# Performance work log

Measured on AMD Instinct MI355X. Metric: run time of the kernel, lower is better.

The kernel has to match this reference:

```python
import jax, jax.numpy as jnp
import numpy as np

B_, N, C, H = 8192, 49, 192, 6
HD = C // H
SCALE = HD ** -0.5


def setup_inputs() -> dict:
    key = jax.random.key(0)
    k0, k1, k2, k3 = jax.random.split(key, 4)
    x = jax.random.normal(k0, (B_, N, C), dtype=jnp.float32)
    mask = jax.random.randint(k1, (B_, N), 0, 2, dtype=jnp.int32)
    w_qkv = jax.random.normal(k2, (C, 3 * C), dtype=jnp.float32) * 0.02
    b_qkv = jnp.zeros((3 * C,), dtype=jnp.float32)
    w_proj = jax.random.normal(k3, (C, C), dtype=jnp.float32) * 0.02
    b_proj = jnp.zeros((C,), dtype=jnp.float32)
    return {"x": x, "mask": mask, "w_qkv": w_qkv, "b_qkv": b_qkv,
            "w_proj": w_proj, "b_proj": b_proj}


def reference(x, mask, w_qkv, b_qkv, w_proj, b_proj):
    # qkv projection: [B_, N, 3C] -> [3, B_, H, N, HD]
    qkv = (x @ w_qkv + b_qkv).reshape(B_, N, 3, H, HD).transpose(2, 0, 3, 1, 4)
    q, k, v = qkv[0], qkv[1], qkv[2]
    # scaled QK^T: [B_, H, N, N]
    attn = jnp.einsum('bhnd,bhmd->bhnm', q, k) * SCALE
    # additive key mask: mask==0 positions get -inf
    attn = jnp.where(mask[:, None, None, :] == 0, -jnp.inf, attn)
    p = jax.nn.softmax(attn, axis=-1)  # dropout p=0 -> identity
    out = jnp.einsum('bhnm,bhmd->bhnd', p, v)  # AV
    out = out.transpose(0, 2, 1, 3).reshape(B_, N, C)
    return out @ w_proj + b_proj
```

## Files before the change

kernel.cpp:

```cpp
#include <hip/hip_runtime.h>


typedef __attribute__((ext_vector_type(8))) short short8;
typedef __attribute__((ext_vector_type(4))) float f32x4;

#define SCALE 0.17677669529663687f

__device__ __forceinline__ unsigned short f2bf(float x) {
    union { float f; unsigned int i; } v; v.f = x;
    return (unsigned short)((v.i + 0x7FFFu + ((v.i >> 16) & 1u)) >> 16);
}

__global__ void repack_qkv_kernel(const float* __restrict__ w,
                                  unsigned short* __restrict__ wp) {
    int idx = blockIdx.x * 256 + threadIdx.x;
    if (idx >= 6 * 576 * 32) return;
    int kk  = idx & 31;
    int col = (idx >> 5) % 576;
    int kt  = idx / (576 * 32);
    wp[idx] = f2bf(w[(kt * 32 + kk) * 576 + col]);
}

__global__ void repack_proj_kernel(const float* __restrict__ w,
                                   unsigned short* __restrict__ wp) {
    int idx = blockIdx.x * 256 + threadIdx.x;
    if (idx >= 6 * 192 * 32) return;
    int kk  = idx & 31;
    int col = (idx >> 5) % 192;
    int kt  = idx / (192 * 32);
    wp[idx] = f2bf(w[(kt * 32 + kk) * 192 + col]);
}

__global__ __launch_bounds__(384)
void win_attn_kernel(const float* __restrict__ x,
                     const int* __restrict__ mask,
                     const float* __restrict__ bqkv,
                     const float* __restrict__ bproj,
                     const unsigned short* __restrict__ wq,
                     const unsigned short* __restrict__ wpj,
                     float* __restrict__ out) {
    __shared__ __align__(16) unsigned short region[44544];
    __shared__ float mbias[64];

    const int b    = blockIdx.x;
    const int tid  = threadIdx.x;
    const int lane = tid & 63;
    const int h    = tid >> 6;
    const int quad = lane >> 4;
    const int l16  = lane & 15;

    const float* xb = x + (size_t)b * 9408;
    for (int i4 = tid; i4 < 2352; i4 += 384) {
        int flat = i4 * 4;
        int n = flat / 192, c = flat % 192;
        float4 v = *(const float4*)(const void*)&xb[flat];
        ushort4 pk = make_ushort4(f2bf(v.x), f2bf(v.y), f2bf(v.z), f2bf(v.w));
        *(ushort4*)(void*)&region[n * 200 + c] = pk;
    }
    if (tid < 375) {
        uint4 z = {0u, 0u, 0u, 0u};
        *(uint4*)(void*)&region[9800 + tid * 8] = z;
    }
    if (tid < 64)
        mbias[tid] = (tid < 49 && mask[b * 49 + tid] != 0) ? 0.0f : -1e30f;
    __syncthreads();

    f32x4 acc[6][4];
    #pragma unroll
    for (int t = 0; t < 6; ++t)
        #pragma unroll
        for (int mt = 0; mt < 4; ++mt)
            acc[t][mt] = (f32x4){0.f, 0.f, 0.f, 0.f};

    int colb[6];
    #pragma unroll
    for (int t = 0; t < 6; ++t) colb[t] = (t >> 1) * 192 + h * 32 + (t & 1) * 16;

    #pragma unroll
    for (int kt = 0; kt < 6; ++kt) {
        short8 af[4];
        #pragma unroll
        for (int mt = 0; mt < 4; ++mt)
            af[mt] = *(const short8*)(const void*)
                     &region[(mt * 16 + l16) * 200 + kt * 32 + quad * 8];
        #pragma unroll
        for (int t = 0; t < 6; ++t) {
            short8 bw = *(const short8*)(const void*)
                        &wq[(size_t)(kt * 576 + colb[t] + l16) * 32 + quad * 8];
            #pragma unroll
            for (int mt = 0; mt < 4; ++mt)
                acc[t][mt] = __builtin_amdgcn_mfma_f32_16x16x32_bf16(
                                 af[mt], bw, acc[t][mt], 0, 0, 0);
        }
    }
    #pragma unroll
    for (int t = 0; t < 6; ++t) {
        float bv = bqkv[colb[t] + l16];
        #pragma unroll
        for (int mt = 0; mt < 4; ++mt)
            #pragma unroll
            for (int r = 0; r < 4; ++r)
                acc[t][mt][r] += bv;
    }
    __syncthreads();

    unsigned short* qb  = &region[h * 7424];
    unsigned short* kb  = qb + 2560;
    unsigned short* vtb = qb + 5120;
    #pragma unroll
    for (int t = 0; t < 2; ++t)
        #pragma unroll
        for (int mt = 0; mt < 4; ++mt)
            #pragma unroll
            for (int r = 0; r < 4; ++r) {
                int row = mt * 16 + quad * 4 + r;
                qb[row * 40 + t * 16 + l16] = f2bf(acc[t    ][mt][r]);
                kb[row * 40 + t * 16 + l16] = f2bf(acc[t + 2][mt][r]);
            }
    #pragma unroll
    for (int t = 0; t < 2; ++t)
        #pragma unroll
        for (int mt = 0; mt < 4; ++mt) {
            int d = t * 16 + l16;
            ushort4 pk = make_ushort4(f2bf(acc[4 + t][mt][0]), f2bf(acc[4 + t][mt][1]),
                                      f2bf(acc[4 + t][mt][2]), f2bf(acc[4 + t][mt][3]));
            *(ushort4*)(void*)&vtb[d * 72 + mt * 16 + quad * 4] = pk;
        }

    f32x4 s[4][4];
    #pragma unroll
    for (int mt = 0; mt < 4; ++mt)
        #pragma unroll
        for (int nt = 0; nt < 4; ++nt)
            s[mt][nt] = (f32x4){0.f, 0.f, 0.f, 0.f};

    {
        short8 aq[4], bk[4];
        #pragma unroll
        for (int mt = 0; mt < 4; ++mt)
            aq[mt] = *(const short8*)(const void*)&qb[(mt * 16 + l16) * 40 + quad * 8];
        #pragma unroll
        for (int nt = 0; nt < 4; ++nt)
            bk[nt] = *(const short8*)(const void*)&kb[(nt * 16 + l16) * 40 + quad * 8];
        #pragma unroll
        for (int mt = 0; mt < 4; ++mt)
            #pragma unroll
            for (int nt = 0; nt < 4; ++nt)
                s[mt][nt] = __builtin_amdgcn_mfma_f32_16x16x32_bf16(
                                aq[mt], bk[nt], s[mt][nt], 0, 0, 0);
    }

    float mb[4];
    #pragma unroll
    for (int nt = 0; nt < 4; ++nt) mb[nt] = mbias[nt * 16 + l16];

    #pragma unroll
    for (int mt = 0; mt < 4; ++mt) {
        #pragma unroll
        for (int r = 0; r < 4; ++r) {
            float v0 = s[mt][0][r] * SCALE + mb[0];
            float v1 = s[mt][1][r] * SCALE + mb[1];
            float v2 = s[mt][2][r] * SCALE + mb[2];
            float v3 = s[mt][3][r] * SCALE + mb[3];
            float mx = fmaxf(fmaxf(v0, v1), fmaxf(v2, v3));
            mx = fmaxf(mx, __shfl_xor(mx, 1));
            mx = fmaxf(mx, __shfl_xor(mx, 2));
            mx = fmaxf(mx, __shfl_xor(mx, 4));
            mx = fmaxf(mx, __shfl_xor(mx, 8));
            float e0 = __expf(v0 - mx), e1 = __expf(v1 - mx);
            float e2 = __expf(v2 - mx), e3 = __expf(v3 - mx);
            float sum = e0 + e1 + e2 + e3;
            sum += __shfl_xor(sum, 1);
            sum += __shfl_xor(sum, 2);
            sum += __shfl_xor(sum, 4);
            sum += __shfl_xor(sum, 8);
            float inv = 1.0f / sum;
            s[mt][0][r] = e0 * inv; s[mt][1][r] = e1 * inv;
            s[mt][2][r] = e2 * inv; s[mt][3][r] = e3 * inv;
        }
    }

    unsigned short* pb = qb;
    #pragma unroll
    for (int mt = 0; mt < 4; ++mt)
        #pragma unroll
        for (int nt = 0; nt < 4; ++nt)
            #pragma unroll
            for (int r = 0; r < 4; ++r)
                pb[(mt * 16 + quad * 4 + r) * 72 + nt * 16 + l16] = f2bf(s[mt][nt][r]);

    f32x4 o[4][2];
    #pragma unroll
    for (int mt = 0; mt < 4; ++mt)
        #pragma unroll
        for (int dt = 0; dt < 2; ++dt)
            o[mt][dt] = (f32x4){0.f, 0.f, 0.f, 0.f};

    #pragma unroll
    for (int kt = 0; kt < 2; ++kt) {
        short8 ap[4], bv[2];
        #pragma unroll
        for (int mt = 0; mt < 4; ++mt)
            ap[mt] = *(const short8*)(const void*)
                     &pb[(mt * 16 + l16) * 72 + kt * 32 + quad * 8];
        #pragma unroll
        for (int dt = 0; dt < 2; ++dt)
            bv[dt] = *(const short8*)(const void*)
                     &vtb[(dt * 16 + l16) * 72 + kt * 32 + quad * 8];
        #pragma unroll
        for (int mt = 0; mt < 4; ++mt)
            #pragma unroll
            for (int dt = 0; dt < 2; ++dt)
                o[mt][dt] = __builtin_amdgcn_mfma_f32_16x16x32_bf16(
                                ap[mt], bv[dt], o[mt][dt], 0, 0, 0);
    }

    __syncthreads();
    #pragma unroll
    for (int dt = 0; dt < 2; ++dt)
        #pragma unroll
        for (int mt = 0; mt < 4; ++mt)
            #pragma unroll
            for (int r = 0; r < 4; ++r)
                region[(mt * 16 + quad * 4 + r) * 200 + h * 32 + dt * 16 + l16]
                    = f2bf(o[mt][dt][r]);
    __syncthreads();

    f32x4 po[2][4];
    #pragma unroll
    for (int nt = 0; nt < 2; ++nt)
        #pragma unroll
        for (int mt = 0; mt < 4; ++mt)
            po[nt][mt] = (f32x4){0.f, 0.f, 0.f, 0.f};

    #pragma unroll
    for (int kt = 0; kt < 6; ++kt) {
        short8 ao[4];
        #pragma unroll
        for (int mt = 0; mt < 4; ++mt)
            ao[mt] = *(const short8*)(const void*)
                     &region[(mt * 16 + l16) * 200 + kt * 32 + quad * 8];
        #pragma unroll
        for (int nt = 0; nt < 2; ++nt) {
            int col = h * 32 + nt * 16 + l16;
            short8 bw = *(const short8*)(const void*)
                        &wpj[(size_t)(kt * 192 + col) * 32 + quad * 8];
            #pragma unroll
            for (int mt = 0; mt < 4; ++mt)
                po[nt][mt] = __builtin_amdgcn_mfma_f32_16x16x32_bf16(
                                 ao[mt], bw, po[nt][mt], 0, 0, 0);
        }
    }

    #pragma unroll
    for (int nt = 0; nt < 2; ++nt) {
        int col = h * 32 + nt * 16 + l16;
        float bv = bproj[col];
        #pragma unroll
        for (int mt = 0; mt < 4; ++mt)
            #pragma unroll
            for (int r = 0; r < 4; ++r) {
                int row = mt * 16 + quad * 4 + r;
                if (row < 49)
                    out[(size_t)b * 9408 + row * 192 + col] = po[nt][mt][r] + bv;
            }
    }
}

extern "C" void kernel_launch(void* const* d_in, const int* in_sizes, int n_in,
                              void* d_out, int out_size, void* d_ws, size_t ws_size,
                              hipStream_t stream) {
    const float* x      = (const float*)d_in[0];
    const int*   mask   = (const int*)d_in[1];
    const float* w_qkv  = (const float*)d_in[2];
    const float* b_qkv  = (const float*)d_in[3];
    const float* w_proj = (const float*)d_in[4];
    const float* b_proj = (const float*)d_in[5];
    float*       out    = (float*)d_out;

    unsigned short* wq_pack = (unsigned short*)d_ws;
    unsigned short* wp_pack = wq_pack + 110592;

    repack_qkv_kernel <<<(110592 + 255) / 256, 256, 0, stream>>>(w_qkv,  wq_pack);
    repack_proj_kernel<<<( 36864 + 255) / 256, 256, 0, stream>>>(w_proj, wp_pack);
    win_attn_kernel<<<8192, 384, 0, stream>>>(x, mask, b_qkv, b_proj,
                                              wq_pack, wp_pack, out);
}
```

Measured before the change: 946.4 us.

## Swizzle per-head LDS buffers, shrink shared memory, merge weight repack kernels

Replaces the padded row strides (40 and 72) for the Q, K, V^T and P tiles with XOR-swizzled unpadded layouts. This cuts the LDS footprint from about 89KB to about 74KB per block, and adds a launch-bounds hint of 3 blocks per CU. The two weight-repack kernels are merged into one launch to save launch overhead. The swizzle must keep 16-byte vector accesses bank-conflict-free, and a tighter register budget could cause spills.

```diff
diff --git a/kernel.cpp b/kernel.cpp
--- a/kernel.cpp
+++ b/kernel.cpp
@@ -11,27 +11,35 @@
     return (unsigned short)((v.i + 0x7FFFu + ((v.i >> 16) & 1u)) >> 16);
 }
 
-__global__ void repack_qkv_kernel(const float* __restrict__ w,
-                                  unsigned short* __restrict__ wp) {
+__device__ __forceinline__ int swz32(int row, int col) {
+    return row * 32 + ((((col >> 3) ^ (row & 3)) << 3) | (col & 7));
+}
+__device__ __forceinline__ int swz64(int row, int col) {
+    return row * 64 + ((((col >> 3) ^ (row & 7)) << 3) | (col & 7));
+}
+
+__global__ void repack_kernel(const float* __restrict__ wqkv,
+                              const float* __restrict__ wproj,
+                              unsigned short* __restrict__ wq_pack,
+                              unsigned short* __restrict__ wp_pack) {
     int idx = blockIdx.x * 256 + threadIdx.x;
-    if (idx >= 6 * 576 * 32) return;
-    int kk  = idx & 31;
-    int col = (idx >> 5) % 576;
-    int kt  = idx / (576 * 32);
-    wp[idx] = f2bf(w[(kt * 32 + kk) * 576 + col]);
-}
-
-__global__ void repack_proj_kernel(const float* __restrict__ w,
-                                   unsigned short* __restrict__ wp) {
-    int idx = blockIdx.x * 256 + threadIdx.x;
-    if (idx >= 6 * 192 * 32) return;
-    int kk  = idx & 31;
-    int col = (idx >> 5) % 192;
-    int kt  = idx / (192 * 32);
-    wp[idx] = f2bf(w[(kt * 32 + kk) * 192 + col]);
-}
-
-__global__ __launch_bounds__(384)
+    if (idx < 6 * 576 * 32) {
+        int kk  = idx & 31;
+        int col = (idx >> 5) % 576;
+        int kt  = idx / (576 * 32);
+        wq_pack[idx] = f2bf(wqkv[(kt * 32 + kk) * 576 + col]);
+    } else {
+        int j = idx - 6 * 576 * 32;
+        if (j < 6 * 192 * 32) {
+            int kk  = j & 31;
+            int col = (j >> 5) % 192;
+            int kt  = j / (192 * 32);
+            wp_pack[j] = f2bf(wproj[(kt * 32 + kk) * 192 + col]);
+        }
+    }
+}
+
+__global__ __launch_bounds__(384, 3)
 void win_attn_kernel(const float* __restrict__ x,
                      const int* __restrict__ mask,
                      const float* __restrict__ bqkv,
@@ -39,7 +47,7 @@
                      const unsigned short* __restrict__ wq,
                      const unsigned short* __restrict__ wpj,
                      float* __restrict__ out) {
-    __shared__ __align__(16) unsigned short region[44544];
+    __shared__ __align__(16) unsigned short region[36864];
     __shared__ float mbias[64];
 
     const int b    = blockIdx.x;
@@ -104,9 +112,9 @@
     }
     __syncthreads();
 
-    unsigned short* qb  = &region[h * 7424];
-    unsigned short* kb  = qb + 2560;
-    unsigned short* vtb = qb + 5120;
+    unsigned short* qb  = &region[h * 6144];
+    unsigned short* kb  = qb + 2048;
+    unsigned short* vtb = qb + 4096;
     #pragma unroll
     for (int t = 0; t < 2; ++t)
         #pragma unroll
@@ -114,8 +122,8 @@
             #pragma unroll
             for (int r = 0; r < 4; ++r) {
                 int row = mt * 16 + quad * 4 + r;
-                qb[row * 40 + t * 16 + l16] = f2bf(acc[t    ][mt][r]);
-                kb[row * 40 + t * 16 + l16] = f2bf(acc[t + 2][mt][r]);
+                qb[swz32(row, t * 16 + l16)] = f2bf(acc[t    ][mt][r]);
+                kb[swz32(row, t * 16 + l16)] = f2bf(acc[t + 2][mt][r]);
             }
     #pragma unroll
     for (int t = 0; t < 2; ++t)
@@ -124,7 +132,7 @@
             int d = t * 16 + l16;
             ushort4 pk = make_ushort4(f2bf(acc[4 + t][mt][0]), f2bf(acc[4 + t][mt][1]),
                                       f2bf(acc[4 + t][mt][2]), f2bf(acc[4 + t][mt][3]));
-            *(ushort4*)(void*)&vtb[d * 72 + mt * 16 + quad * 4] = pk;
+            *(ushort4*)(void*)&vtb[swz64(d, mt * 16 + quad * 4)] = pk;
         }
 
     f32x4 s[4][4];
@@ -138,10 +146,10 @@
         short8 aq[4], bk[4];
         #pragma unroll
         for (int mt = 0; mt < 4; ++mt)
-            aq[mt] = *(const short8*)(const void*)&qb[(mt * 16 + l16) * 40 + quad * 8];
+            aq[mt] = *(const short8*)(const void*)&qb[swz32(mt * 16 + l16, quad * 8)];
         #pragma unroll
         for (int nt = 0; nt < 4; ++nt)
-            bk[nt] = *(const short8*)(const void*)&kb[(nt * 16 + l16) * 40 + quad * 8];
+            bk[nt] = *(const short8*)(const void*)&kb[swz32(nt * 16 + l16, quad * 8)];
         #pragma unroll
         for (int mt = 0; mt < 4; ++mt)
             #pragma unroll
@@ -187,7 +195,7 @@
         for (int nt = 0; nt < 4; ++nt)
             #pragma unroll
             for (int r = 0; r < 4; ++r)
-                pb[(mt * 16 + quad * 4 + r) * 72 + nt * 16 + l16] = f2bf(s[mt][nt][r]);
+                pb[swz64(mt * 16 + quad * 4 + r, nt * 16 + l16)] = f2bf(s[mt][nt][r]);
 
     f32x4 o[4][2];
     #pragma unroll
@@ -202,11 +210,11 @@
         #pragma unroll
         for (int mt = 0; mt < 4; ++mt)
             ap[mt] = *(const short8*)(const void*)
-                     &pb[(mt * 16 + l16) * 72 + kt * 32 + quad * 8];
+                     &pb[swz64(mt * 16 + l16, kt * 32 + quad * 8)];
         #pragma unroll
         for (int dt = 0; dt < 2; ++dt)
             bv[dt] = *(const short8*)(const void*)
-                     &vtb[(dt * 16 + l16) * 72 + kt * 32 + quad * 8];
+                     &vtb[swz64(dt * 16 + l16, kt * 32 + quad * 8)];
         #pragma unroll
         for (int mt = 0; mt < 4; ++mt)
             #pragma unroll
@@ -281,8 +289,8 @@
     unsigned short* wq_pack = (unsigned short*)d_ws;
     unsigned short* wp_pack = wq_pack + 110592;
 
-    repack_qkv_kernel <<<(110592 + 255) / 256, 256, 0, stream>>>(w_qkv,  wq_pack);
-    repack_proj_kernel<<<( 36864 + 255) / 256, 256, 0, stream>>>(w_proj, wp_pack);
+    repack_kernel<<<(110592 + 36864 + 255) / 256, 256, 0, stream>>>(
+        w_qkv, w_proj, wq_pack, wp_pack);
     win_attn_kernel<<<8192, 384, 0, stream>>>(x, mask, b_qkv, b_proj,
                                               wq_pack, wp_pack, out);
 }
```

Measured after the change: 993.7 us. 1.05x slower.
